# Optimization experiments

Measured on AMD Instinct MI355X. Metric: run time of the kernel, lower is better.

Reference implementation:

```python
import jax, jax.numpy as jnp
import numpy as np

T, B, D, H = 256, 64, 1024, 1024
EPS = 0.01  # perturbation scale (epsilon in create_new_Vs_mage)


def setup_inputs() -> dict:
    key = jax.random.key(0)
    k = jax.random.split(key, 6)
    scale = 1.0 / np.sqrt(H)  # torch LSTM default init scale
    return {
        "x": jax.random.normal(k[0], (T, B, D), dtype=jnp.float32),
        "g": jax.random.normal(k[1], (T, B, 4 * H), dtype=jnp.float32),
        "W_ih": jax.random.normal(k[2], (4 * H, D), dtype=jnp.float32) * scale,
        "W_hh": jax.random.normal(k[3], (4 * H, H), dtype=jnp.float32) * scale,
        "b_ih": jax.random.normal(k[4], (4 * H,), dtype=jnp.float32) * scale,
        "b_hh": jax.random.normal(k[5], (4 * H,), dtype=jnp.float32) * scale,
    }


def reference(x, g, W_ih, W_hh, b_ih, b_hh):
    """Manual per-timestep LSTM with MAGE forward-gradient tangent propagation.

    Per step the perturbation of each gate's weights is rank-1:
      vW_ih_k = g_k (x_t/norm)^T, vW_hh_k = g_k (h/norm)^T,
      norm = sqrt(|x|^2 + |h|^2 + 2),
    with gate/bias sharing exactly as in create_new_Vs_mage. The tangent
    contribution vW_ih_k @ x_t is then g_k * |x|^2/norm, etc., so we never
    materialize the [B, H, D] perturbation matrices.
    """
    Bsz = x.shape[1]
    Hd = W_hh.shape[1]

    def step(carry, inp):
        h, c, dh, dc = carry
        x_t, g_t = inp  # [B, D], [B, 4H]
        # primal gate preactivations
        pre = x_t @ W_ih.T + b_ih + h @ W_hh.T + b_hh  # [B, 4H]
        pi, pf, pg, po = jnp.split(pre, 4, axis=1)
        i = jax.nn.sigmoid(pi)
        f = jax.nn.sigmoid(pf)
        gg = jnp.tanh(pg)
        o = jax.nn.sigmoid(po)
        # MAGE rank-1 perturbation tangents
        norm = jnp.sqrt((x_t ** 2).sum(1, keepdims=True)
                        + (h ** 2).sum(1, keepdims=True) + 2.0)  # [B, 1]
        s = (norm * norm - 2.0) / norm   # (|x|^2 + |h|^2) / norm
        inv = 1.0 / norm
        g0, g1, g2, g3 = jnp.split(g_t * EPS, 4, axis=1)
        dpre_h = dh @ W_hh.T  # tangent through recurrent weights, [B, 4H]
        dhi, dhf, dhg, dho = jnp.split(dpre_h, 4, axis=1)
        # bias pairing per create_new_Vs_mage: vb_ii=g0/n, vb_hi=g1/n,
        # vb_if=g2/n, vb_hf=g3/n, vb_ig=vb_ii, vb_hg=vb_hi, vb_io=vb_if, vb_ho=vb_hf
        dpi = g0 * (s + inv) + g1 * inv + dhi
        dpf = g1 * s + (g2 + g3) * inv + dhf
        dpg = g2 * s + (g0 + g1) * inv + dhg
        dpo = g3 * s + (g2 + g3) * inv + dho
        di = i * (1.0 - i) * dpi
        df = f * (1.0 - f) * dpf
        dgg = (1.0 - gg * gg) * dpg
        do = o * (1.0 - o) * dpo
        c2 = f * c + i * gg
        dc2 = df * c + f * dc + di * gg + i * dgg
        tc = jnp.tanh(c2)
        h2 = o * tc
        dh2 = do * tc + o * (1.0 - tc * tc) * dc2
        return (h2, c2, dh2, dc2), (h2, dh2)

    z = jnp.zeros((Bsz, Hd), dtype=x.dtype)
    _, (hs, dhs) = jax.lax.scan(step, (z, z, z, z), (x, g))
    return jnp.stack([hs, dhs], axis=0)  # [2, T, B, H]
```

## Files before the change

### kernel.cpp

```cpp
#include <hip/hip_runtime.h>
#include <hip/hip_bf16.h>

typedef unsigned short u16;
typedef unsigned int u32;
typedef unsigned long long u64;
typedef __attribute__((ext_vector_type(8))) short short8;
typedef __attribute__((ext_vector_type(4))) float floatx4;

#define EPS 0.01f

#define OFF_FLAGS  (0ull)
#define OFF_HPART  (4096ull)
#define OFF_HD     (40960ull)
#define OFF_XNORM  (565248ull)

__device__ __forceinline__ u16 f2b(float v) {
  __hip_bfloat16 b = __float2bfloat16(v);
  return *reinterpret_cast<u16*>(&b);
}
__device__ __forceinline__ float b2f(u16 u) {
  u32 x = ((u32)u) << 16;
  return __uint_as_float(x);
}
__device__ __forceinline__ float halfsel(float w, int hi) {
  u32 u = __float_as_uint(w);
  return b2f((u16)(hi ? (u >> 16) : (u & 0xffffu)));
}
__device__ __forceinline__ float sigm(float x) { return 1.0f / (1.0f + __expf(-x)); }
__device__ __forceinline__ float tanh_(float x) { return 2.0f / (1.0f + __expf(-2.0f * x)) - 1.0f; }

__device__ __forceinline__ u64 ld_sys_u64(const u64* p) {
  return __hip_atomic_load(p, __ATOMIC_RELAXED, __HIP_MEMORY_SCOPE_SYSTEM);
}


__global__ void xnorm_kernel(const float* __restrict__ x, float* __restrict__ xn) {
  const int wid = threadIdx.x >> 6, lane = threadIdx.x & 63;
  const int row = blockIdx.x * 4 + wid;
  const float4* p = (const float4*)(x + (size_t)row * 1024);
  float s = 0.f;
  #pragma unroll
  for (int i = 0; i < 4; ++i) {
    float4 v = p[lane + i * 64];
    s += v.x * v.x + v.y * v.y + v.z * v.z + v.w * v.w;
  }
  for (int o = 32; o; o >>= 1) s += __shfl_down(s, o);
  if (lane == 0) xn[row] = s;
}

#define LDA 88
__global__ __launch_bounds__(256) void pregemm_kernel(const float* __restrict__ A,
                                                      const float* __restrict__ Bw,
                                                      const float* __restrict__ bih,
                                                      const float* __restrict__ bhh,
                                                      u16* __restrict__ O) {
  __shared__ u16 Al[128 * LDA];
  __shared__ u16 Bl[128 * LDA];
  const int tid = threadIdx.x, lane = tid & 63, wid = tid >> 6;
  const int bm = blockIdx.x & 127, bn = blockIdx.x >> 7;
  const size_t m0 = (size_t)bm * 128, n0 = (size_t)bn * 128;
  const int wrow = (wid & 1) * 64, wcol = (wid >> 1) * 64;
  const int lrow = lane & 15, lko = (lane >> 4) * 8;
  floatx4 acc[4][4];
  #pragma unroll
  for (int i = 0; i < 4; ++i)
    #pragma unroll
    for (int j = 0; j < 4; ++j) acc[i][j] = (floatx4)(0.0f);

  for (int k0 = 0; k0 < 1024; k0 += 64) {
    __syncthreads();
    #pragma unroll
    for (int i = 0; i < 8; ++i) {
      int cid = tid + i * 256;
      int row = cid >> 4;
      int kc = cid & 15;
      float4 va = *(const float4*)&A[(m0 + row) * 1024 + k0 + kc * 4];
      ushort4 oa;
      oa.x = f2b(va.x); oa.y = f2b(va.y); oa.z = f2b(va.z); oa.w = f2b(va.w);
      *(ushort4*)&Al[row * LDA + kc * 4] = oa;
      float4 vb = *(const float4*)&Bw[(n0 + row) * 1024 + k0 + kc * 4];
      ushort4 ob;
      ob.x = f2b(vb.x); ob.y = f2b(vb.y); ob.z = f2b(vb.z); ob.w = f2b(vb.w);
      *(ushort4*)&Bl[row * LDA + kc * 4] = ob;
    }
    __syncthreads();
    #pragma unroll
    for (int ks = 0; ks < 2; ++ks) {
      short8 af[4], bf[4];
      #pragma unroll
      for (int i = 0; i < 4; ++i)
        af[i] = *(const short8*)&Al[(wrow + i * 16 + lrow) * LDA + ks * 32 + lko];
      #pragma unroll
      for (int j = 0; j < 4; ++j)
        bf[j] = *(const short8*)&Bl[(wcol + j * 16 + lrow) * LDA + ks * 32 + lko];
      #pragma unroll
      for (int i = 0; i < 4; ++i)
        #pragma unroll
        for (int j = 0; j < 4; ++j)
          acc[i][j] = __builtin_amdgcn_mfma_f32_16x16x32_bf16(af[i], bf[j], acc[i][j], 0, 0, 0);
    }
  }
  #pragma unroll
  for (int j = 0; j < 4; ++j) {
    const size_t col = n0 + wcol + j * 16 + lrow;
    const float bv = bih[col] + bhh[col];
    const size_t q = col >> 10;
    const size_t jt = (col & 1023) >> 4;
    const size_t jj = col & 15;
    const size_t cbase = ((q >= 2) ? 33554432ull : 0ull) + jt * 32 + (q & 1) * 16 + jj;
    #pragma unroll
    for (int i = 0; i < 4; ++i) {
      const size_t rowb = m0 + wrow + i * 16 + (lane >> 4) * 4;
      #pragma unroll
      for (int r = 0; r < 4; ++r) O[cbase + (rowb + r) * 2048] = f2b(acc[i][j][r] + bv);
    }
  }
}

__global__ __launch_bounds__(256, 1) void recurrent_kernel(
    const float* __restrict__ gin, const float* __restrict__ whh,
    const float* __restrict__ xnorm2, u32* hd, float* hpart, int* flags, float* out) {
  extern __shared__ char smem[];
  u16* Wlds = (u16*)smem;
  float* rbuf = (float*)(smem + 132096);

  const int tid = threadIdx.x, lane = tid & 63, wid = tid >> 6;
  const int grp = blockIdx.x & 3, jt = blockIdx.x >> 2;
  const int lrow = lane & 15, hv = lane >> 4, lko = hv * 8;
  const int j = jt * 16 + lrow;
  const int bloc = hv * 4 + wid;

  #pragma unroll
  for (int it = 0; it < 64; ++it) {
    int cid = tid + it * 256;
    int rowl = cid >> 8;
    int kc = cid & 255;
    int q = rowl >> 4, jj = rowl & 15;
    size_t grow = (size_t)q * 1024 + (size_t)jt * 16 + jj;
    float4 v = *(const float4*)&whh[grow * 1024 + kc * 4];
    ushort4 o;
    o.x = f2b(v.x); o.y = f2b(v.y); o.z = f2b(v.z); o.w = f2b(v.w);
    *(ushort4*)&Wlds[rowl * 1032 + kc * 4] = o;
  }
  __syncthreads();

  float cr = 0.f, dcr = 0.f;

  for (int t = 0; t < 256; ++t) {
    const int p = t & 1, p2 = p ^ 1;
    const size_t m = (size_t)t * 64 + grp * 16 + bloc;

    float gv[4];
    #pragma unroll
    for (int q = 0; q < 4; ++q) gv[q] = EPS * gin[m * 4096 + (size_t)q * 1024 + j];
    const size_t fb = m * 1024 + (size_t)jt * 16 + (lrow >> 1);
    float pw0 = out[fb];
    float pw1 = out[fb + 8];
    float pw2 = out[16777216ull + fb];
    float pw3 = out[16777216ull + fb + 8];
    float xnv = xnorm2[m];
    asm volatile("" ::: "memory");

    floatx4 acc[2][4];
    #pragma unroll
    for (int m2 = 0; m2 < 2; ++m2)
      #pragma unroll
      for (int q = 0; q < 4; ++q) acc[m2][q] = (floatx4)(0.0f);

    float hn = 0.f;
    if (t > 0) {
      for (int it = 0; it < 4000000; ++it) {
        int v = __hip_atomic_load(&flags[grp * 64 + lane], __ATOMIC_RELAXED,
                                  __HIP_MEMORY_SCOPE_SYSTEM);
        if (lane == jt) v = 0x7fffffff;
        if (__all(v >= t)) break;
        __builtin_amdgcn_s_sleep(1);
      }
      asm volatile("" ::: "memory");

      {
        const u64* hp = (const u64*)(hpart + ((size_t)(p * 4 + grp) * 16 + bloc) * 64 + lrow * 4);
        u64 q0 = ld_sys_u64(hp), q1 = ld_sys_u64(hp + 1);
        float s = __uint_as_float((u32)q0) + __uint_as_float((u32)(q0 >> 32)) +
                  __uint_as_float((u32)q1) + __uint_as_float((u32)(q1 >> 32));
        s += __shfl_xor(s, 1);
        s += __shfl_xor(s, 2);
        s += __shfl_xor(s, 4);
        s += __shfl_xor(s, 8);
        hn = s;
      }

      const u32* hdrow = hd + ((size_t)(p * 4 + grp)) * 16384 + (size_t)lrow * 1024;
      const int kb = wid * 256 + lko;
      u64 A0 = ld_sys_u64((const u64*)(hdrow + kb));
      u64 A1 = ld_sys_u64((const u64*)(hdrow + kb + 2));
      u64 A2 = ld_sys_u64((const u64*)(hdrow + kb + 4));
      u64 A3 = ld_sys_u64((const u64*)(hdrow + kb + 6));
      #pragma unroll
      for (int ks = 0; ks < 8; ++ks) {
        u64 N0 = A0, N1 = A1, N2 = A2, N3 = A3;
        if (ks < 7) {
          const int nb = kb + (ks + 1) * 32;
          N0 = ld_sys_u64((const u64*)(hdrow + nb));
          N1 = ld_sys_u64((const u64*)(hdrow + nb + 2));
          N2 = ld_sys_u64((const u64*)(hdrow + nb + 4));
          N3 = ld_sys_u64((const u64*)(hdrow + nb + 6));
        }
        u32 w[8] = {(u32)A0, (u32)(A0 >> 32), (u32)A1, (u32)(A1 >> 32),
                    (u32)A2, (u32)(A2 >> 32), (u32)A3, (u32)(A3 >> 32)};
        short8 a0, a1;
        #pragma unroll
        for (int i = 0; i < 8; ++i) {
          a0[i] = (short)(w[i] & 0xffffu);
          a1[i] = (short)(w[i] >> 16);
        }
        const int k0 = wid * 256 + ks * 32;
        #pragma unroll
        for (int q = 0; q < 4; ++q) {
          short8 bq = *(const short8*)&Wlds[(q * 16 + lrow) * 1032 + k0 + lko];
          acc[0][q] = __builtin_amdgcn_mfma_f32_16x16x32_bf16(a0, bq, acc[0][q], 0, 0, 0);
          acc[1][q] = __builtin_amdgcn_mfma_f32_16x16x32_bf16(a1, bq, acc[1][q], 0, 0, 0);
        }
        A0 = N0; A1 = N1; A2 = N2; A3 = N3;
      }
    }

    float fin[2][4] = {{0.f, 0.f, 0.f, 0.f}, {0.f, 0.f, 0.f, 0.f}};
    if (t > 0) {
      __syncthreads();
      #pragma unroll
      for (int m2 = 0; m2 < 2; ++m2)
        #pragma unroll
        for (int q = 0; q < 4; ++q)
          #pragma unroll
          for (int s2 = 0; s2 < 3; ++s2) {
            int r = s2 + (s2 >= wid ? 1 : 0);
            rbuf[((((m2 * 4 + q) * 4 + wid) * 3 + s2) << 6) + lane] = acc[m2][q][r];
          }
      __syncthreads();
      #pragma unroll
      for (int m2 = 0; m2 < 2; ++m2)
        #pragma unroll
        for (int q = 0; q < 4; ++q) {
          float sfin = acc[m2][q][wid];
          #pragma unroll
          for (int w2 = 0; w2 < 4; ++w2)
            if (w2 != wid) {
              int slot = wid - (wid > w2 ? 1 : 0);
              sfin += rbuf[((((m2 * 4 + q) * 4 + w2) * 3 + slot) << 6) + lane];
            }
          fin[m2][q] = sfin;
        }
    }

    {
      const int hi = lrow & 1;
      float pre0 = halfsel(pw0, hi), pre1 = halfsel(pw1, hi);
      float pre2 = halfsel(pw2, hi), pre3 = halfsel(pw3, hi);
      float sum2 = xnv + hn;
      float nrm = sqrtf(sum2 + 2.0f);
      float inv = 1.0f / nrm;
      float s_ = sum2 * inv;
      float pv0 = fin[0][0] + pre0, pv1 = fin[0][1] + pre1;
      float pv2 = fin[0][2] + pre2, pv3 = fin[0][3] + pre3;
      float d0 = gv[0] * (s_ + inv) + gv[1] * inv + fin[1][0];
      float d1 = gv[1] * s_ + (gv[2] + gv[3]) * inv + fin[1][1];
      float d2 = gv[2] * s_ + (gv[0] + gv[1]) * inv + fin[1][2];
      float d3 = gv[3] * s_ + (gv[2] + gv[3]) * inv + fin[1][3];
      float iv = sigm(pv0), fv = sigm(pv1), gg = tanh_(pv2), ov = sigm(pv3);
      float di = iv * (1.f - iv) * d0;
      float df = fv * (1.f - fv) * d1;
      float dgg = (1.f - gg * gg) * d2;
      float dov = ov * (1.f - ov) * d3;
      float c2 = fv * cr + iv * gg;
      float dc2 = df * cr + fv * dcr + di * gg + iv * dgg;
      float tc = tanh_(c2);
      float h2 = ov * tc;
      float dh2 = dov * tc + ov * (1.f - tc * tc) * dc2;
      cr = c2;
      dcr = dc2;
      out[m * 1024 + j] = h2;
      out[16777216ull + m * 1024 + j] = dh2;
      u32 packv = (u32)f2b(h2) | ((u32)f2b(dh2) << 16);
      __hip_atomic_store(&hd[((size_t)(p2 * 4 + grp)) * 16384 + (size_t)bloc * 1024 + j],
                         packv, __ATOMIC_RELAXED, __HIP_MEMORY_SCOPE_SYSTEM);
      float v2 = h2 * h2;
      v2 += __shfl_xor(v2, 1);
      v2 += __shfl_xor(v2, 2);
      v2 += __shfl_xor(v2, 4);
      v2 += __shfl_xor(v2, 8);
      if (lrow == 0)
        __hip_atomic_store(&hpart[((size_t)(p2 * 4 + grp) * 16 + bloc) * 64 + jt],
                           v2, __ATOMIC_RELAXED, __HIP_MEMORY_SCOPE_SYSTEM);
    }
    __syncthreads();
    if (tid == 0)
      __hip_atomic_store(&flags[grp * 64 + jt], t + 1, __ATOMIC_RELAXED,
                         __HIP_MEMORY_SCOPE_SYSTEM);
  }
}

extern "C" void kernel_launch(void* const* d_in, const int* in_sizes, int n_in,
                              void* d_out, int out_size, void* d_ws, size_t ws_size,
                              hipStream_t stream) {
  const float* x = (const float*)d_in[0];
  const float* g = (const float*)d_in[1];
  const float* wih = (const float*)d_in[2];
  const float* whh = (const float*)d_in[3];
  const float* bih = (const float*)d_in[4];
  const float* bhh = (const float*)d_in[5];
  char* ws = (char*)d_ws;
  int* flags = (int*)(ws + OFF_FLAGS);
  float* hpart = (float*)(ws + OFF_HPART);
  u32* hd = (u32*)(ws + OFF_HD);
  float* xn = (float*)(ws + OFF_XNORM);
  float* out = (float*)d_out;

  xnorm_kernel<<<4096, 256, 0, stream>>>(x, xn);
  pregemm_kernel<<<4096, 256, 0, stream>>>(x, wih, bih, bhh, (u16*)d_out);
  hipFuncSetAttribute((const void*)recurrent_kernel,
                      hipFuncAttributeMaxDynamicSharedMemorySize, 156672);
  recurrent_kernel<<<256, 256, 156672, stream>>>(g, whh, xn, hd, hpart, flags, out);
}
```

Baseline: 2.637 ms.

## Per-wave flag polling, batched hd loads, perm unpacking, deferred hpart read

Result: slower. 3.074 ms (+16.6%).

```diff
diff --git a/kernel.cpp b/kernel.cpp
--- a/kernel.cpp
+++ b/kernel.cpp
@@ -129,6 +129,7 @@
   const int lrow = lane & 15, hv = lane >> 4, lko = hv * 8;
   const int j = jt * 16 + lrow;
   const int bloc = hv * 4 + wid;
+  const int pj = wid * 16 + lrow;
 
   #pragma unroll
   for (int it = 0; it < 64; ++it) {
@@ -167,52 +168,35 @@
       #pragma unroll
       for (int q = 0; q < 4; ++q) acc[m2][q] = (floatx4)(0.0f);
 
-    float hn = 0.f;
     if (t > 0) {
       for (int it = 0; it < 4000000; ++it) {
-        int v = __hip_atomic_load(&flags[grp * 64 + lane], __ATOMIC_RELAXED,
+        int v = __hip_atomic_load(&flags[grp * 64 + pj], __ATOMIC_RELAXED,
                                   __HIP_MEMORY_SCOPE_SYSTEM);
-        if (lane == jt) v = 0x7fffffff;
+        if (pj == jt) v = 0x7fffffff;
         if (__all(v >= t)) break;
         __builtin_amdgcn_s_sleep(1);
       }
       asm volatile("" ::: "memory");
 
-      {
-        const u64* hp = (const u64*)(hpart + ((size_t)(p * 4 + grp) * 16 + bloc) * 64 + lrow * 4);
-        u64 q0 = ld_sys_u64(hp), q1 = ld_sys_u64(hp + 1);
-        float s = __uint_as_float((u32)q0) + __uint_as_float((u32)(q0 >> 32)) +
-                  __uint_as_float((u32)q1) + __uint_as_float((u32)(q1 >> 32));
-        s += __shfl_xor(s, 1);
-        s += __shfl_xor(s, 2);
-        s += __shfl_xor(s, 4);
-        s += __shfl_xor(s, 8);
-        hn = s;
+      const u32* hdrow = hd + ((size_t)(p * 4 + grp)) * 16384 + (size_t)lrow * 1024;
+      u64 Abuf[32];
+      #pragma unroll
+      for (int ks = 0; ks < 8; ++ks) {
+        const int kb = wid * 256 + ks * 32 + lko;
+        Abuf[4 * ks + 0] = ld_sys_u64((const u64*)(hdrow + kb));
+        Abuf[4 * ks + 1] = ld_sys_u64((const u64*)(hdrow + kb + 2));
+        Abuf[4 * ks + 2] = ld_sys_u64((const u64*)(hdrow + kb + 4));
+        Abuf[4 * ks + 3] = ld_sys_u64((const u64*)(hdrow + kb + 6));
       }
-
-      const u32* hdrow = hd + ((size_t)(p * 4 + grp)) * 16384 + (size_t)lrow * 1024;
-      const int kb = wid * 256 + lko;
-      u64 A0 = ld_sys_u64((const u64*)(hdrow + kb));
-      u64 A1 = ld_sys_u64((const u64*)(hdrow + kb + 2));
-      u64 A2 = ld_sys_u64((const u64*)(hdrow + kb + 4));
-      u64 A3 = ld_sys_u64((const u64*)(hdrow + kb + 6));
       #pragma unroll
       for (int ks = 0; ks < 8; ++ks) {
-        u64 N0 = A0, N1 = A1, N2 = A2, N3 = A3;
-        if (ks < 7) {
-          const int nb = kb + (ks + 1) * 32;
-          N0 = ld_sys_u64((const u64*)(hdrow + nb));
-          N1 = ld_sys_u64((const u64*)(hdrow + nb + 2));
-          N2 = ld_sys_u64((const u64*)(hdrow + nb + 4));
-          N3 = ld_sys_u64((const u64*)(hdrow + nb + 6));
-        }
-        u32 w[8] = {(u32)A0, (u32)(A0 >> 32), (u32)A1, (u32)(A1 >> 32),
-                    (u32)A2, (u32)(A2 >> 32), (u32)A3, (u32)(A3 >> 32)};
         short8 a0, a1;
         #pragma unroll
-        for (int i = 0; i < 8; ++i) {
-          a0[i] = (short)(w[i] & 0xffffu);
-          a1[i] = (short)(w[i] >> 16);
+        for (int i = 0; i < 4; ++i) {
+          u32 lo = (u32)Abuf[4 * ks + i];
+          u32 hi2 = (u32)(Abuf[4 * ks + i] >> 32);
+          ((u32*)&a0)[i] = __builtin_amdgcn_perm(hi2, lo, 0x05040100u);
+          ((u32*)&a1)[i] = __builtin_amdgcn_perm(hi2, lo, 0x07060302u);
         }
         const int k0 = wid * 256 + ks * 32;
         #pragma unroll
@@ -221,13 +205,12 @@
           acc[0][q] = __builtin_amdgcn_mfma_f32_16x16x32_bf16(a0, bq, acc[0][q], 0, 0, 0);
           acc[1][q] = __builtin_amdgcn_mfma_f32_16x16x32_bf16(a1, bq, acc[1][q], 0, 0, 0);
         }
-        A0 = N0; A1 = N1; A2 = N2; A3 = N3;
       }
     }
 
     float fin[2][4] = {{0.f, 0.f, 0.f, 0.f}, {0.f, 0.f, 0.f, 0.f}};
+    float hn = 0.f;
     if (t > 0) {
-      __syncthreads();
       #pragma unroll
       for (int m2 = 0; m2 < 2; ++m2)
         #pragma unroll
@@ -238,6 +221,8 @@
             rbuf[((((m2 * 4 + q) * 4 + wid) * 3 + s2) << 6) + lane] = acc[m2][q][r];
           }
       __syncthreads();
+      const u64* hp = (const u64*)(hpart + ((size_t)(p * 4 + grp) * 16 + bloc) * 64 + lrow * 4);
+      u64 q0 = ld_sys_u64(hp), q1 = ld_sys_u64(hp + 1);
       #pragma unroll
       for (int m2 = 0; m2 < 2; ++m2)
         #pragma unroll
@@ -251,6 +236,13 @@
             }
           fin[m2][q] = sfin;
         }
+      float s = __uint_as_float((u32)q0) + __uint_as_float((u32)(q0 >> 32)) +
+                __uint_as_float((u32)q1) + __uint_as_float((u32)(q1 >> 32));
+      s += __shfl_xor(s, 1);
+      s += __shfl_xor(s, 2);
+      s += __shfl_xor(s, 4);
+      s += __shfl_xor(s, 8);
+      hn = s;
     }
 
     {
```
